# Kernel tuning notes

Hardware: AMD Instinct MI355X
Metric: run time of the kernel (lower is better)

## Reference

```python
import jax, jax.numpy as jnp
import numpy as np

B, D, K, C = 512, 256, 65536, 1000
T_SUP, T_DC, LS = 0.07, 0.1, 0.1
EPS = 1e-8


def _l2norm(x, axis):
    return x / jnp.linalg.norm(x, axis=axis, keepdims=True)


def setup_inputs() -> dict:
    key = jax.random.key(0)
    k1, k2, k3, k4, k5, k6, k7, k8 = jax.random.split(key, 8)
    norm_q = _l2norm(jax.random.normal(k1, (B, D), jnp.float32), axis=1)
    k_feat = _l2norm(jax.random.normal(k2, (B, D), jnp.float32), axis=1)
    q_logits = jax.random.normal(k3, (B, C), jnp.float32)
    logits_k = jax.random.normal(k4, (B, C), jnp.float32)
    queue = _l2norm(jax.random.normal(k5, (D, K), jnp.float32), axis=0)
    # queue_label_prob stores softmaxed class-probabilities column-wise (prob.T)
    queue_label_prob = jax.nn.softmax(jax.random.normal(k6, (C, K), jnp.float32), axis=0)
    queue_label = jax.random.randint(k7, (K,), 0, C, jnp.int64)
    target = jax.random.randint(k8, (B,), 0, C, jnp.int64)
    return {
        "norm_q": norm_q, "q_logits": q_logits, "k_feat": k_feat,
        "logits_k": logits_k, "queue": queue,
        "queue_label_prob": queue_label_prob, "queue_label": queue_label,
        "target": target, "knn_k": 200,
    }


def reference(norm_q, q_logits, k_feat, logits_k, queue, queue_label_prob,
              queue_label, target, knn_k):
    b = norm_q.shape[0]

    # ---- supcon_in ----
    sim = norm_q @ queue                                  # [B, K]
    _, idx = jax.lax.top_k(sim, knn_k)                    # [B, knn_k]
    sim_knn = jnp.take_along_axis(sim, idx, axis=1)
    w = jax.nn.softmax(sim_knn / T_SUP, axis=-1)
    pos = (target[:, None] == queue_label[idx])           # [B, knn_k]
    gt = jnp.sum(w * pos, axis=1)                         # [B]
    m = gt > EPS
    supin_loss = jnp.sum(jnp.where(m, -jnp.log(jnp.where(m, gt, 1.0)), 0.0)) / b

    # ---- label-smoothed onehot ----
    onehot = jnp.full((b, C), LS / (C - 1), jnp.float32)
    onehot = onehot.at[jnp.arange(b), target].set(1.0 - LS)

    log_q = jax.nn.log_softmax(q_logits, axis=1)
    q_mask = jax.nn.softmax(q_logits, axis=1).min(axis=1) > EPS  # [B]

    # ---- fc loss (masked CE with label smoothing) ----
    fc_loss = -jnp.sum(jnp.sum(onehot * log_q, axis=1) * q_mask) / b

    # ---- generate_dc_target (no-grad in original) ----
    sim_k = jax.nn.softmax((k_feat @ queue) / T_DC, axis=-1)      # [B, K]
    dc_target = sim_k @ queue_label_prob.T                        # [B, C]

    # ---- dc loss: KL(dc_target || softmax(q_logits)), masked, sum / B ----
    kl = jnp.where(dc_target > 0, dc_target * (jnp.log(jnp.where(dc_target > 0, dc_target, 1.0)) - log_q), 0.0)
    dc_loss = jnp.sum(jnp.sum(kl, axis=1) * q_mask) / b

    return (supin_loss, fc_loss, dc_loss)
```

## Files before the change

kernel.cpp:

```cpp
#include <hip/hip_runtime.h>
#include <math.h>

#define BN 512
#define DN 256
#define KN 65536
#define CN 1000
#define EQ_CAP 512
#define EPSTR 136

typedef __attribute__((ext_vector_type(8))) short bf16x8;
typedef __attribute__((ext_vector_type(4))) float f32x4;

__device__ __forceinline__ unsigned short f2bf(float f) {
    unsigned u = __float_as_uint(f);
    unsigned r = (u + 0x7FFFu + ((u >> 16) & 1u)) >> 16;
    return (unsigned short)r;
}
__device__ __forceinline__ float bf2f(unsigned short h) {
    return __uint_as_float(((unsigned)h) << 16);
}
__device__ __forceinline__ unsigned fkey16(unsigned b) {
    b &= 0xFFFFu;
    return (b & 0x8000u) ? ((~b) & 0xFFFFu) : (b | 0x8000u);
}
__device__ __forceinline__ void async16(const void* g, void* l) {
    __builtin_amdgcn_global_load_lds(
        (const __attribute__((address_space(1))) unsigned*)g,
        (__attribute__((address_space(3))) unsigned*)l, 16, 0, 0);
}

__global__ void __launch_bounds__(256) cvt_bf16(const float* __restrict__ in,
                                                unsigned short* __restrict__ out) {
    int i = (blockIdx.x * 256 + threadIdx.x) * 4;
    float4 v = *(const float4*)&in[i];
    ushort4 o;
    o.x = f2bf(v.x); o.y = f2bf(v.y); o.z = f2bf(v.z); o.w = f2bf(v.w);
    *(ushort4*)&out[i] = o;
}

__global__ void __launch_bounds__(256) transpose_q(const float* __restrict__ Q,
                                                   unsigned short* __restrict__ Qt) {
    __shared__ float T[64][65];
    int tid = threadIdx.x;
    int n0 = blockIdx.x * 64;
    int d0 = blockIdx.y * 64;
    #pragma unroll
    for (int i = 0; i < 4; ++i) {
        int flat = i * 256 + tid;
        int d = flat >> 4, nq = (flat & 15) * 4;
        float4 v = *(const float4*)&Q[(size_t)(d0 + d) * KN + n0 + nq];
        T[d][nq] = v.x; T[d][nq + 1] = v.y; T[d][nq + 2] = v.z; T[d][nq + 3] = v.w;
    }
    __syncthreads();
    int n = tid >> 2, dbase = (tid & 3) * 16;
    unsigned u[8];
    #pragma unroll
    for (int j = 0; j < 8; ++j) {
        unsigned short a = f2bf(T[dbase + 2 * j][n]);
        unsigned short b = f2bf(T[dbase + 2 * j + 1][n]);
        u[j] = (unsigned)a | ((unsigned)b << 16);
    }
    unsigned short* o = &Qt[(size_t)(n0 + n) * DN + d0 + dbase];
    *(uint4*)o = make_uint4(u[0], u[1], u[2], u[3]);
    *(uint4*)(o + 8) = make_uint4(u[4], u[5], u[6], u[7]);
}

__global__ void __launch_bounds__(256) gemm_sim(const unsigned short* __restrict__ A,
                                                const unsigned short* __restrict__ Bt,
                                                unsigned short* __restrict__ simOut,
                                                unsigned short* __restrict__ expOut,
                                                float* __restrict__ Zb,
                                                int mBlockSplit) {
    __shared__ unsigned short smem[128 * 64 * 2];
    __shared__ float Zred[128];
    unsigned short* As = smem;
    unsigned short* Bs = smem + 128 * 64;
    int tid = threadIdx.x;
    int n0 = blockIdx.x * 128, m0 = blockIdx.y * 128;
    bool isExp = ((int)blockIdx.y >= mBlockSplit);
    int lane = tid & 63, w = tid >> 6;
    int l15 = lane & 15, quad = lane >> 4;
    int wm = w & 1, wn = w >> 1;
    f32x4 acc[4][4];
    #pragma unroll
    for (int mi = 0; mi < 4; ++mi)
        #pragma unroll
        for (int ni = 0; ni < 4; ++ni)
            #pragma unroll
            for (int j = 0; j < 4; ++j) acc[mi][ni][j] = 0.f;

    for (int k0 = 0; k0 < DN; k0 += 64) {
        #pragma unroll
        for (int i = 0; i < 4; ++i) {
            int f = (i * 256 + tid) * 8;
            async16(A + (size_t)(m0 + (f >> 6)) * DN + k0 + (f & 63), &As[f]);
        }
        #pragma unroll
        for (int i = 0; i < 4; ++i) {
            int f = (i * 256 + tid) * 8;
            async16(Bt + (size_t)(n0 + (f >> 6)) * DN + k0 + (f & 63), &Bs[f]);
        }
        __syncthreads();
        #pragma unroll
        for (int ks = 0; ks < 2; ++ks) {
            bf16x8 am[4], bn[4];
            #pragma unroll
            for (int mi = 0; mi < 4; ++mi)
                am[mi] = *(const bf16x8*)&As[(wm * 64 + mi * 16 + l15) * 64 + ks * 32 + quad * 8];
            #pragma unroll
            for (int ni = 0; ni < 4; ++ni)
                bn[ni] = *(const bf16x8*)&Bs[(wn * 64 + ni * 16 + l15) * 64 + ks * 32 + quad * 8];
            #pragma unroll
            for (int mi = 0; mi < 4; ++mi)
                #pragma unroll
                for (int ni = 0; ni < 4; ++ni)
                    acc[mi][ni] = __builtin_amdgcn_mfma_f32_16x16x32_bf16(bn[ni], am[mi], acc[mi][ni], 0, 0, 0);
        }
        __syncthreads();
    }

    unsigned short* obase = isExp ? expOut : simOut;
    int orow0 = isExp ? (m0 - mBlockSplit * 128) : m0;
    float rsum[4] = {0.f, 0.f, 0.f, 0.f};

    #pragma unroll
    for (int round = 0; round < 2; ++round) {
        if (wm == round) {
            #pragma unroll
            for (int mi = 0; mi < 4; ++mi) {
                int mrow = mi * 16 + l15;
                #pragma unroll
                for (int ni = 0; ni < 4; ++ni) {
                    int nc = wn * 64 + ni * 16 + quad * 4;
                    float v0 = acc[mi][ni][0], v1 = acc[mi][ni][1];
                    float v2 = acc[mi][ni][2], v3 = acc[mi][ni][3];
                    if (isExp) {
                        v0 = __expf(v0 * 10.0f); v1 = __expf(v1 * 10.0f);
                        v2 = __expf(v2 * 10.0f); v3 = __expf(v3 * 10.0f);
                    }
                    unsigned short u0 = f2bf(v0), u1 = f2bf(v1), u2 = f2bf(v2), u3 = f2bf(v3);
                    if (isExp) rsum[mi] += bf2f(u0) + bf2f(u1) + bf2f(u2) + bf2f(u3);
                    *(uint2*)&smem[mrow * EPSTR + nc] =
                        make_uint2((unsigned)u0 | ((unsigned)u1 << 16),
                                   (unsigned)u2 | ((unsigned)u3 << 16));
                }
            }
        }
        __syncthreads();
        #pragma unroll
        for (int j = 0; j < 4; ++j) {
            int fc = j * 256 + tid;
            int mr = fc >> 4;
            int ch = fc & 15;
            uint4 val = *(uint4*)&smem[mr * EPSTR + ch * 8];
            int g = orow0 + round * 64 + mr;
            *(uint4*)&obase[(size_t)g * KN + n0 + ch * 8] = val;
        }
        __syncthreads();
    }

    if (isExp) {
        float v4[4];
        #pragma unroll
        for (int mi = 0; mi < 4; ++mi) {
            float v = rsum[mi];
            v += __shfl_xor(v, 16, 64);
            v += __shfl_xor(v, 32, 64);
            v4[mi] = v;
        }
        if (wn == 0 && quad == 0) {
            #pragma unroll
            for (int mi = 0; mi < 4; ++mi) Zred[wm * 64 + mi * 16 + l15] = v4[mi];
        }
        __syncthreads();
        if (wn == 1 && quad == 0) {
            #pragma unroll
            for (int mi = 0; mi < 4; ++mi) Zred[wm * 64 + mi * 16 + l15] += v4[mi];
        }
        __syncthreads();
        if (tid < 128) atomicAdd(&Zb[orow0 + tid], Zred[tid]);
    }
}

__global__ void __launch_bounds__(256) supcon(const unsigned short* __restrict__ sim,
                                              const int* __restrict__ qlabel,
                                              const int* __restrict__ target,
                                              const int* __restrict__ knnp,
                                              float* __restrict__ out0) {
    __shared__ unsigned hist[4][256];
    __shared__ unsigned s_sel, s_cntAbove;
    __shared__ int eqIdx[EQ_CAP];
    __shared__ unsigned eqCount;
    __shared__ float redZ[256], redN[256];
    int tid = threadIdx.x, w = tid >> 6;
    int row = blockIdx.x;
    const unsigned short* srow = sim + (size_t)row * KN;
    int knn = *knnp;
    int tgt = target[row];
    if (tid == 0) { eqCount = 0u; }
    #pragma unroll
    for (int j = 0; j < 4; ++j) hist[j][tid] = 0u;
    __syncthreads();
    for (int i0 = tid * 4; i0 < KN; i0 += 1024) {
        uint2 v = *(const uint2*)&srow[i0];
        atomicAdd(&hist[w][fkey16(v.x) >> 8], 1u);
        atomicAdd(&hist[w][fkey16(v.x >> 16) >> 8], 1u);
        atomicAdd(&hist[w][fkey16(v.y) >> 8], 1u);
        atomicAdd(&hist[w][fkey16(v.y >> 16) >> 8], 1u);
    }
    __syncthreads();
    if (tid == 0) {
        unsigned acc = 0; int chosen = 0;
        for (int bin = 255; bin >= 0; --bin) {
            unsigned h = hist[0][bin] + hist[1][bin] + hist[2][bin] + hist[3][bin];
            if (acc + h >= (unsigned)knn) { chosen = bin; break; }
            acc += h;
        }
        s_cntAbove = acc; s_sel = (unsigned)chosen;
    }
    __syncthreads();
    unsigned selHi = s_sel;
    #pragma unroll
    for (int j = 0; j < 4; ++j) hist[j][tid] = 0u;
    __syncthreads();
    for (int i0 = tid * 4; i0 < KN; i0 += 1024) {
        uint2 v = *(const uint2*)&srow[i0];
        unsigned k0 = fkey16(v.x), k1 = fkey16(v.x >> 16), k2 = fkey16(v.y), k3 = fkey16(v.y >> 16);
        if ((k0 >> 8) == selHi) atomicAdd(&hist[w][k0 & 255u], 1u);
        if ((k1 >> 8) == selHi) atomicAdd(&hist[w][k1 & 255u], 1u);
        if ((k2 >> 8) == selHi) atomicAdd(&hist[w][k2 & 255u], 1u);
        if ((k3 >> 8) == selHi) atomicAdd(&hist[w][k3 & 255u], 1u);
    }
    __syncthreads();
    if (tid == 0) {
        unsigned acc = s_cntAbove; int chosen = 0;
        for (int bin = 255; bin >= 0; --bin) {
            unsigned h = hist[0][bin] + hist[1][bin] + hist[2][bin] + hist[3][bin];
            if (acc + h >= (unsigned)knn) { chosen = bin; break; }
            acc += h;
        }
        s_cntAbove = acc; s_sel = (selHi << 8) | (unsigned)chosen;
    }
    __syncthreads();
    unsigned tu = s_sel;
    unsigned cgt = s_cntAbove;
    const float invT = 1.0f / 0.07f;
    float Zl = 0.f, Nl = 0.f;
    for (int i0 = tid * 4; i0 < KN; i0 += 1024) {
        uint2 v = *(const uint2*)&srow[i0];
        unsigned bits[4] = {v.x & 0xFFFFu, v.x >> 16, v.y & 0xFFFFu, v.y >> 16};
        #pragma unroll
        for (int j = 0; j < 4; ++j) {
            unsigned u = fkey16(bits[j]);
            if (u > tu) {
                float e = __expf(bf2f((unsigned short)bits[j]) * invT);
                Zl += e;
                if (qlabel[i0 + j] == tgt) Nl += e;
            } else if (u == tu) {
                unsigned pos = atomicAdd(&eqCount, 1u);
                if (pos < EQ_CAP) eqIdx[pos] = i0 + j;
            }
        }
    }
    redZ[tid] = Zl; redN[tid] = Nl;
    __syncthreads();
    for (int s = 128; s > 0; s >>= 1) {
        if (tid < s) { redZ[tid] += redZ[tid + s]; redN[tid] += redN[tid + s]; }
        __syncthreads();
    }
    if (tid == 0) {
        float Z = redZ[0], num = redN[0];
        int neq = (int)(eqCount < (unsigned)EQ_CAP ? eqCount : (unsigned)EQ_CAP);
        int needed = knn - (int)cgt;
        if (needed > neq) needed = neq;
        for (int a = 1; a < neq; ++a) {
            int v = eqIdx[a]; int b2 = a - 1;
            while (b2 >= 0 && eqIdx[b2] > v) { eqIdx[b2 + 1] = eqIdx[b2]; --b2; }
            eqIdx[b2 + 1] = v;
        }
        unsigned tb = (tu & 0x8000u) ? (tu & 0x7FFFu) : ((~tu) & 0xFFFFu);
        float wt = __expf(bf2f((unsigned short)tb) * invT);
        for (int a = 0; a < needed; ++a) {
            Z += wt;
            if (qlabel[eqIdx[a]] == tgt) num += wt;
        }
        float gt = num / Z;
        if (gt > 1e-8f) atomicAdd(out0, -logf(gt) * (1.0f / (float)BN));
    }
}

__global__ void __launch_bounds__(256) dc_gemm(const unsigned short* __restrict__ E,
                                               const float* __restrict__ P,
                                               float* __restrict__ dct) {
    __shared__ unsigned short As[128 * 32];
    __shared__ unsigned short Bs[128 * 32];
    int tid = threadIdx.x;
    int c0 = blockIdx.x * 128, m0 = blockIdx.y * 128;
    int kb = blockIdx.z * (KN / 16);
    int lane = tid & 63, w = tid >> 6;
    int l15 = lane & 15, quad = lane >> 4;
    int wm = w & 1, wn = w >> 1;
    int crow = tid >> 1, khalf = (tid & 1) * 16;
    bool cvalid = (c0 + crow) < CN;
    const float* pbase = P + (size_t)(c0 + crow) * KN + khalf;
    f32x4 acc[4][4];
    #pragma unroll
    for (int r = 0; r < 4; ++r)
        #pragma unroll
        for (int c = 0; c < 4; ++c)
            #pragma unroll
            for (int j = 0; j < 4; ++j) acc[r][c][j] = 0.f;
    for (int kc = 0; kc < KN / 16; kc += 32) {
        int k0 = kb + kc;
        #pragma unroll
        for (int i = 0; i < 2; ++i) {
            int flat = (i * 256 + tid) * 8;
            int row = flat >> 5, kk = flat & 31;
            async16(E + (size_t)(m0 + row) * KN + k0 + kk, &As[flat]);
        }
        float4 p0 = make_float4(0.f, 0.f, 0.f, 0.f), p1 = p0, p2 = p0, p3 = p0;
        if (cvalid) {
            p0 = *(const float4*)&pbase[k0];
            p1 = *(const float4*)&pbase[k0 + 4];
            p2 = *(const float4*)&pbase[k0 + 8];
            p3 = *(const float4*)&pbase[k0 + 12];
        }
        unsigned u0 = (unsigned)f2bf(p0.x) | ((unsigned)f2bf(p0.y) << 16);
        unsigned u1 = (unsigned)f2bf(p0.z) | ((unsigned)f2bf(p0.w) << 16);
        unsigned u2 = (unsigned)f2bf(p1.x) | ((unsigned)f2bf(p1.y) << 16);
        unsigned u3 = (unsigned)f2bf(p1.z) | ((unsigned)f2bf(p1.w) << 16);
        unsigned u4 = (unsigned)f2bf(p2.x) | ((unsigned)f2bf(p2.y) << 16);
        unsigned u5 = (unsigned)f2bf(p2.z) | ((unsigned)f2bf(p2.w) << 16);
        unsigned u6 = (unsigned)f2bf(p3.x) | ((unsigned)f2bf(p3.y) << 16);
        unsigned u7 = (unsigned)f2bf(p3.z) | ((unsigned)f2bf(p3.w) << 16);
        *(uint4*)&Bs[crow * 32 + khalf] = make_uint4(u0, u1, u2, u3);
        *(uint4*)&Bs[crow * 32 + khalf + 8] = make_uint4(u4, u5, u6, u7);
        __syncthreads();
        bf16x8 af[4], bfr[4];
        #pragma unroll
        for (int r = 0; r < 4; ++r) af[r] = *(const bf16x8*)&As[(wm * 64 + r * 16 + l15) * 32 + quad * 8];
        #pragma unroll
        for (int c = 0; c < 4; ++c) bfr[c] = *(const bf16x8*)&Bs[(wn * 64 + c * 16 + l15) * 32 + quad * 8];
        #pragma unroll
        for (int r = 0; r < 4; ++r)
            #pragma unroll
            for (int c = 0; c < 4; ++c)
                acc[r][c] = __builtin_amdgcn_mfma_f32_16x16x32_bf16(af[r], bfr[c], acc[r][c], 0, 0, 0);
        __syncthreads();
    }
    #pragma unroll
    for (int r = 0; r < 4; ++r)
        #pragma unroll
        for (int reg = 0; reg < 4; ++reg) {
            int m = m0 + wm * 64 + r * 16 + quad * 4 + reg;
            #pragma unroll
            for (int c = 0; c < 4; ++c) {
                int cc = c0 + wn * 64 + c * 16 + l15;
                atomicAdd(&dct[m * 1024 + cc], acc[r][c][reg]);
            }
        }
}

__global__ void __launch_bounds__(256) logq_fc(const float* __restrict__ x_all,
                                               const int* __restrict__ target,
                                               float* __restrict__ logq,
                                               float* __restrict__ qmask,
                                               float* __restrict__ out1) {
    int row = blockIdx.x, tid = threadIdx.x;
    const float* x = x_all + (size_t)row * CN;
    __shared__ float red[256], red2[256];
    float mx = -INFINITY, mn = INFINITY;
    for (int c = tid; c < CN; c += 256) { float v = x[c]; mx = fmaxf(mx, v); mn = fminf(mn, v); }
    red[tid] = mx; red2[tid] = mn;
    __syncthreads();
    for (int s = 128; s > 0; s >>= 1) {
        if (tid < s) { red[tid] = fmaxf(red[tid], red[tid + s]); red2[tid] = fminf(red2[tid], red2[tid + s]); }
        __syncthreads();
    }
    mx = red[0]; mn = red2[0];
    __syncthreads();
    float se = 0.f, sx = 0.f;
    for (int c = tid; c < CN; c += 256) { float v = x[c]; se += __expf(v - mx); sx += v; }
    red[tid] = se; red2[tid] = sx;
    __syncthreads();
    for (int s = 128; s > 0; s >>= 1) {
        if (tid < s) { red[tid] += red[tid + s]; red2[tid] += red2[tid + s]; }
        __syncthreads();
    }
    float lse = mx + logf(red[0]);
    float sumlogq = red2[0] - (float)CN * lse;
    for (int c = tid; c < CN; c += 256) logq[(size_t)row * CN + c] = x[c] - lse;
    if (tid == 0) {
        float lqt = x[target[row]] - lse;
        bool qm = (mn - lse) > logf(1e-8f);
        qmask[row] = qm ? 1.0f : 0.0f;
        if (qm) {
            float fc = -(0.1f / 999.0f * (sumlogq - lqt) + 0.9f * lqt);
            atomicAdd(out1, fc * (1.0f / (float)BN));
        }
    }
}

__global__ void __launch_bounds__(256) dc_loss(const float* __restrict__ dct,
                                               const float* __restrict__ logq,
                                               const float* __restrict__ qmask,
                                               const float* __restrict__ Z,
                                               float* __restrict__ out2) {
    int row = blockIdx.x, tid = threadIdx.x;
    __shared__ float red[256];
    float invZ = 1.0f / Z[row];
    float s = 0.f;
    for (int c = tid; c < CN; c += 256) {
        float T = dct[row * 1024 + c] * invZ;
        if (T > 0.f) s += T * (logf(T) - logq[(size_t)row * CN + c]);
    }
    red[tid] = s;
    __syncthreads();
    for (int st = 128; st > 0; st >>= 1) {
        if (tid < st) red[tid] += red[tid + st];
        __syncthreads();
    }
    if (tid == 0 && qmask[row] > 0.f)
        atomicAdd(out2, red[0] * (1.0f / (float)BN));
}

extern "C" void kernel_launch(void* const* d_in, const int* in_sizes, int n_in,
                              void* d_out, int out_size, void* d_ws, size_t ws_size,
                              hipStream_t stream) {
    (void)in_sizes; (void)n_in; (void)out_size;
    const float* norm_q   = (const float*)d_in[0];
    const float* q_logits = (const float*)d_in[1];
    const float* k_feat   = (const float*)d_in[2];
    const float* queue    = (const float*)d_in[4];
    const float* qlp      = (const float*)d_in[5];
    const int*   qlabel   = (const int*)d_in[6];
    const int*   target   = (const int*)d_in[7];
    const int*   knnp     = (const int*)d_in[8];
    float* out = (float*)d_out;
    char* ws = (char*)d_ws;

    const size_t SIM_B = 67108864;
    const size_t QT_B  = 33554432;
    const size_t AC_B  = 524288;
    const size_t FUSED_NEED = SIM_B * 2 + QT_B + AC_B + 2097152 + 2048 + 2048000 + 2048;
    bool fused = (ws_size >= FUSED_NEED);

    unsigned short *simBF, *Ebf, *queueT, *Acat;
    float *dct, *Zb, *logq, *qmask;
    if (fused) {
        simBF  = (unsigned short*)(ws);
        Ebf    = (unsigned short*)(ws + SIM_B);
        queueT = (unsigned short*)(ws + 2 * SIM_B);
        Acat   = (unsigned short*)(ws + 2 * SIM_B + QT_B);
        dct    = (float*)(ws + 2 * SIM_B + QT_B + AC_B);
    } else {
        simBF  = (unsigned short*)(ws);
        Ebf    = simBF;
        queueT = (unsigned short*)(ws + SIM_B);
        Acat   = (unsigned short*)(ws + SIM_B + QT_B);
        dct    = (float*)(ws + SIM_B + QT_B + AC_B);
    }
    Zb    = (float*)((char*)dct + 2097152);
    logq  = (float*)((char*)Zb + 2048);
    qmask = (float*)((char*)logq + 2048000);

    hipMemsetAsync(dct, 0, 2097152 + 2048, stream);
    hipMemsetAsync(d_out, 0, 3 * sizeof(float), stream);

    cvt_bf16<<<dim3(128), 256, 0, stream>>>(norm_q, Acat);
    cvt_bf16<<<dim3(128), 256, 0, stream>>>(k_feat, Acat + (size_t)BN * DN);
    transpose_q<<<dim3(KN / 64, 4), 256, 0, stream>>>(queue, queueT);

    if (fused) {
        gemm_sim<<<dim3(KN / 128, 8), 256, 0, stream>>>(Acat, queueT, simBF, Ebf, Zb, 4);
        supcon<<<dim3(BN), 256, 0, stream>>>(simBF, qlabel, target, knnp, out + 0);
    } else {
        gemm_sim<<<dim3(KN / 128, 4), 256, 0, stream>>>(Acat, queueT, simBF, nullptr, nullptr, 4);
        supcon<<<dim3(BN), 256, 0, stream>>>(simBF, qlabel, target, knnp, out + 0);
        gemm_sim<<<dim3(KN / 128, 4), 256, 0, stream>>>(Acat + (size_t)BN * DN, queueT,
                                                        nullptr, Ebf, Zb, 0);
    }
    dc_gemm<<<dim3(8, 4, 16), 256, 0, stream>>>(Ebf, qlp, dct);
    logq_fc<<<dim3(BN), 256, 0, stream>>>(q_logits, target, logq, qmask, out + 1);
    dc_loss<<<dim3(BN), 256, 0, stream>>>(dct, logq, qmask, Zb, out + 2);
}
```

Before: 800.9 us.

## Split dc_gemm K into partial buffers and parallelize supcon bin selection

The DC GEMM now splits K into 32 chunks, each writing to its own partial buffer, instead of accumulating into one buffer with float atomics. It uses a 64-wide K tile with XOR-swizzled LDS and register-staged loads. dc_loss sums the 32 partials per element. In supcon, the single-thread serial histogram bin search becomes a parallel suffix scan over the 256 bins. The cost is 64MB of extra partial-buffer traffic, and the non-fused workspace fallback path is removed.

```diff
diff --git a/kernel.cpp b/kernel.cpp
--- a/kernel.cpp
+++ b/kernel.cpp
@@ -7,6 +7,7 @@
 #define CN 1000
 #define EQ_CAP 512
 #define EPSTR 136
+#define DCSPLIT 32
 
 typedef __attribute__((ext_vector_type(8))) short bf16x8;
 typedef __attribute__((ext_vector_type(4))) float f32x4;
@@ -188,6 +189,7 @@
                                               const int* __restrict__ knnp,
                                               float* __restrict__ out0) {
     __shared__ unsigned hist[4][256];
+    __shared__ unsigned sc[256];
     __shared__ unsigned s_sel, s_cntAbove;
     __shared__ int eqIdx[EQ_CAP];
     __shared__ unsigned eqCount;
@@ -195,9 +197,9 @@
     int tid = threadIdx.x, w = tid >> 6;
     int row = blockIdx.x;
     const unsigned short* srow = sim + (size_t)row * KN;
-    int knn = *knnp;
+    unsigned knn = (unsigned)*knnp;
     int tgt = target[row];
-    if (tid == 0) { eqCount = 0u; }
+    if (tid == 0) eqCount = 0u;
     #pragma unroll
     for (int j = 0; j < 4; ++j) hist[j][tid] = 0u;
     __syncthreads();
@@ -209,16 +211,19 @@
         atomicAdd(&hist[w][fkey16(v.y >> 16) >> 8], 1u);
     }
     __syncthreads();
-    if (tid == 0) {
-        unsigned acc = 0; int chosen = 0;
-        for (int bin = 255; bin >= 0; --bin) {
-            unsigned h = hist[0][bin] + hist[1][bin] + hist[2][bin] + hist[3][bin];
-            if (acc + h >= (unsigned)knn) { chosen = bin; break; }
-            acc += h;
-        }
-        s_cntAbove = acc; s_sel = (unsigned)chosen;
-    }
-    __syncthreads();
+    {
+        unsigned tot = hist[0][tid] + hist[1][tid] + hist[2][tid] + hist[3][tid];
+        sc[tid] = tot; __syncthreads();
+        #pragma unroll
+        for (int off = 1; off < 256; off <<= 1) {
+            unsigned v = (tid + off < 256) ? sc[tid + off] : 0u;
+            __syncthreads();
+            sc[tid] += v; __syncthreads();
+        }
+        unsigned S = sc[tid];
+        if (S >= knn && S - tot < knn) { s_sel = (unsigned)tid; s_cntAbove = S - tot; }
+        __syncthreads();
+    }
     unsigned selHi = s_sel;
     #pragma unroll
     for (int j = 0; j < 4; ++j) hist[j][tid] = 0u;
@@ -232,16 +237,23 @@
         if ((k3 >> 8) == selHi) atomicAdd(&hist[w][k3 & 255u], 1u);
     }
     __syncthreads();
-    if (tid == 0) {
-        unsigned acc = s_cntAbove; int chosen = 0;
-        for (int bin = 255; bin >= 0; --bin) {
-            unsigned h = hist[0][bin] + hist[1][bin] + hist[2][bin] + hist[3][bin];
-            if (acc + h >= (unsigned)knn) { chosen = bin; break; }
-            acc += h;
-        }
-        s_cntAbove = acc; s_sel = (selHi << 8) | (unsigned)chosen;
-    }
-    __syncthreads();
+    {
+        unsigned base = s_cntAbove;
+        unsigned tot = hist[0][tid] + hist[1][tid] + hist[2][tid] + hist[3][tid];
+        sc[tid] = tot; __syncthreads();
+        #pragma unroll
+        for (int off = 1; off < 256; off <<= 1) {
+            unsigned v = (tid + off < 256) ? sc[tid + off] : 0u;
+            __syncthreads();
+            sc[tid] += v; __syncthreads();
+        }
+        unsigned S = base + sc[tid];
+        if (S >= knn && S - tot < knn) {
+            s_sel = (selHi << 8) | (unsigned)tid;
+            s_cntAbove = S - tot;
+        }
+        __syncthreads();
+    }
     unsigned tu = s_sel;
     unsigned cgt = s_cntAbove;
     const float invT = 1.0f / 0.07f;
@@ -271,7 +283,7 @@
     if (tid == 0) {
         float Z = redZ[0], num = redN[0];
         int neq = (int)(eqCount < (unsigned)EQ_CAP ? eqCount : (unsigned)EQ_CAP);
-        int needed = knn - (int)cgt;
+        int needed = (int)knn - (int)cgt;
         if (needed > neq) needed = neq;
         for (int a = 1; a < neq; ++a) {
             int v = eqIdx[a]; int b2 = a - 1;
@@ -291,73 +303,72 @@
 
 __global__ void __launch_bounds__(256) dc_gemm(const unsigned short* __restrict__ E,
                                                const float* __restrict__ P,
-                                               float* __restrict__ dct) {
-    __shared__ unsigned short As[128 * 32];
-    __shared__ unsigned short Bs[128 * 32];
+                                               float* __restrict__ part) {
+    __shared__ unsigned short As[128 * 64];
+    __shared__ unsigned short Bs[128 * 64];
     int tid = threadIdx.x;
     int c0 = blockIdx.x * 128, m0 = blockIdx.y * 128;
-    int kb = blockIdx.z * (KN / 16);
+    int kb = blockIdx.z * (KN / DCSPLIT);
     int lane = tid & 63, w = tid >> 6;
     int l15 = lane & 15, quad = lane >> 4;
-    int wm = w & 1, wn = w >> 1;
-    int crow = tid >> 1, khalf = (tid & 1) * 16;
-    bool cvalid = (c0 + crow) < CN;
-    const float* pbase = P + (size_t)(c0 + crow) * KN + khalf;
+    int wm = w & 1, wc = w >> 1;
     f32x4 acc[4][4];
     #pragma unroll
-    for (int r = 0; r < 4; ++r)
-        #pragma unroll
-        for (int c = 0; c < 4; ++c)
-            #pragma unroll
-            for (int j = 0; j < 4; ++j) acc[r][c][j] = 0.f;
-    for (int kc = 0; kc < KN / 16; kc += 32) {
+    for (int ci = 0; ci < 4; ++ci)
+        #pragma unroll
+        for (int mi = 0; mi < 4; ++mi)
+            #pragma unroll
+            for (int j = 0; j < 4; ++j) acc[ci][mi][j] = 0.f;
+
+    for (int kc = 0; kc < KN / DCSPLIT; kc += 64) {
         int k0 = kb + kc;
         #pragma unroll
-        for (int i = 0; i < 2; ++i) {
-            int flat = (i * 256 + tid) * 8;
-            int row = flat >> 5, kk = flat & 31;
-            async16(E + (size_t)(m0 + row) * KN + k0 + kk, &As[flat]);
-        }
-        float4 p0 = make_float4(0.f, 0.f, 0.f, 0.f), p1 = p0, p2 = p0, p3 = p0;
-        if (cvalid) {
-            p0 = *(const float4*)&pbase[k0];
-            p1 = *(const float4*)&pbase[k0 + 4];
-            p2 = *(const float4*)&pbase[k0 + 8];
-            p3 = *(const float4*)&pbase[k0 + 12];
-        }
-        unsigned u0 = (unsigned)f2bf(p0.x) | ((unsigned)f2bf(p0.y) << 16);
-        unsigned u1 = (unsigned)f2bf(p0.z) | ((unsigned)f2bf(p0.w) << 16);
-        unsigned u2 = (unsigned)f2bf(p1.x) | ((unsigned)f2bf(p1.y) << 16);
-        unsigned u3 = (unsigned)f2bf(p1.z) | ((unsigned)f2bf(p1.w) << 16);
-        unsigned u4 = (unsigned)f2bf(p2.x) | ((unsigned)f2bf(p2.y) << 16);
-        unsigned u5 = (unsigned)f2bf(p2.z) | ((unsigned)f2bf(p2.w) << 16);
-        unsigned u6 = (unsigned)f2bf(p3.x) | ((unsigned)f2bf(p3.y) << 16);
-        unsigned u7 = (unsigned)f2bf(p3.z) | ((unsigned)f2bf(p3.w) << 16);
-        *(uint4*)&Bs[crow * 32 + khalf] = make_uint4(u0, u1, u2, u3);
-        *(uint4*)&Bs[crow * 32 + khalf + 8] = make_uint4(u4, u5, u6, u7);
-        __syncthreads();
-        bf16x8 af[4], bfr[4];
-        #pragma unroll
-        for (int r = 0; r < 4; ++r) af[r] = *(const bf16x8*)&As[(wm * 64 + r * 16 + l15) * 32 + quad * 8];
-        #pragma unroll
-        for (int c = 0; c < 4; ++c) bfr[c] = *(const bf16x8*)&Bs[(wn * 64 + c * 16 + l15) * 32 + quad * 8];
-        #pragma unroll
-        for (int r = 0; r < 4; ++r)
-            #pragma unroll
-            for (int c = 0; c < 4; ++c)
-                acc[r][c] = __builtin_amdgcn_mfma_f32_16x16x32_bf16(af[r], bfr[c], acc[r][c], 0, 0, 0);
-        __syncthreads();
-    }
-    #pragma unroll
-    for (int r = 0; r < 4; ++r)
-        #pragma unroll
-        for (int reg = 0; reg < 4; ++reg) {
-            int m = m0 + wm * 64 + r * 16 + quad * 4 + reg;
-            #pragma unroll
-            for (int c = 0; c < 4; ++c) {
-                int cc = c0 + wn * 64 + c * 16 + l15;
-                atomicAdd(&dct[m * 1024 + cc], acc[r][c][reg]);
-            }
+        for (int i = 0; i < 4; ++i) {
+            int f = (i * 256 + tid) * 8;
+            int er = f >> 6, ek = f & 63;
+            uint4 ev = *(const uint4*)&E[(size_t)(m0 + er) * KN + k0 + ek];
+            int cj = (ek >> 3) ^ (er & 7);
+            *(uint4*)&As[er * 64 + cj * 8] = ev;
+        }
+        #pragma unroll
+        for (int i = 0; i < 8; ++i) {
+            int f = (i * 256 + tid) * 4;
+            int pr = f >> 6, pk = f & 63;
+            float4 pv = make_float4(0.f, 0.f, 0.f, 0.f);
+            if (c0 + pr < CN) pv = *(const float4*)&P[(size_t)(c0 + pr) * KN + k0 + pk];
+            unsigned lo = (unsigned)f2bf(pv.x) | ((unsigned)f2bf(pv.y) << 16);
+            unsigned hi = (unsigned)f2bf(pv.z) | ((unsigned)f2bf(pv.w) << 16);
+            int cj = (pk >> 3) ^ (pr & 7);
+            *(uint2*)&Bs[pr * 64 + cj * 8 + (pk & 7)] = make_uint2(lo, hi);
+        }
+        __syncthreads();
+        #pragma unroll
+        for (int ks = 0; ks < 2; ++ks) {
+            int sw = ((ks * 4 + quad) ^ (l15 & 7)) * 8;
+            bf16x8 am[4], bc[4];
+            #pragma unroll
+            for (int mi = 0; mi < 4; ++mi)
+                am[mi] = *(const bf16x8*)&As[(wm * 64 + mi * 16 + l15) * 64 + sw];
+            #pragma unroll
+            for (int ci = 0; ci < 4; ++ci)
+                bc[ci] = *(const bf16x8*)&Bs[(wc * 64 + ci * 16 + l15) * 64 + sw];
+            #pragma unroll
+            for (int ci = 0; ci < 4; ++ci)
+                #pragma unroll
+                for (int mi = 0; mi < 4; ++mi)
+                    acc[ci][mi] = __builtin_amdgcn_mfma_f32_16x16x32_bf16(bc[ci], am[mi], acc[ci][mi], 0, 0, 0);
+        }
+        __syncthreads();
+    }
+    float* pb = part + (size_t)blockIdx.z * (512 * 1024);
+    #pragma unroll
+    for (int ci = 0; ci < 4; ++ci)
+        #pragma unroll
+        for (int mi = 0; mi < 4; ++mi) {
+            int m = m0 + wm * 64 + mi * 16 + l15;
+            int c = c0 + wc * 64 + ci * 16 + quad * 4;
+            *(float4*)&pb[(size_t)m * 1024 + c] =
+                make_float4(acc[ci][mi][0], acc[ci][mi][1], acc[ci][mi][2], acc[ci][mi][3]);
         }
 }
 
@@ -401,7 +412,7 @@
     }
 }
 
-__global__ void __launch_bounds__(256) dc_loss(const float* __restrict__ dct,
+__global__ void __launch_bounds__(256) dc_loss(const float* __restrict__ part,
                                                const float* __restrict__ logq,
                                                const float* __restrict__ qmask,
                                                const float* __restrict__ Z,
@@ -411,7 +422,11 @@
     float invZ = 1.0f / Z[row];
     float s = 0.f;
     for (int c = tid; c < CN; c += 256) {
-        float T = dct[row * 1024 + c] * invZ;
+        float t = 0.f;
+        #pragma unroll
+        for (int sp = 0; sp < DCSPLIT; ++sp)
+            t += part[(size_t)sp * (512 * 1024) + (size_t)row * 1024 + c];
+        float T = t * invZ;
         if (T > 0.f) s += T * (logf(T) - logq[(size_t)row * CN + c]);
     }
     red[tid] = s;
@@ -427,7 +442,7 @@
 extern "C" void kernel_launch(void* const* d_in, const int* in_sizes, int n_in,
                               void* d_out, int out_size, void* d_ws, size_t ws_size,
                               hipStream_t stream) {
-    (void)in_sizes; (void)n_in; (void)out_size;
+    (void)in_sizes; (void)n_in; (void)out_size; (void)ws_size;
     const float* norm_q   = (const float*)d_in[0];
     const float* q_logits = (const float*)d_in[1];
     const float* k_feat   = (const float*)d_in[2];
@@ -439,48 +454,25 @@
     float* out = (float*)d_out;
     char* ws = (char*)d_ws;
 
-    const size_t SIM_B = 67108864;
-    const size_t QT_B  = 33554432;
-    const size_t AC_B  = 524288;
-    const size_t FUSED_NEED = SIM_B * 2 + QT_B + AC_B + 2097152 + 2048 + 2048000 + 2048;
-    bool fused = (ws_size >= FUSED_NEED);
-
-    unsigned short *simBF, *Ebf, *queueT, *Acat;
-    float *dct, *Zb, *logq, *qmask;
-    if (fused) {
-        simBF  = (unsigned short*)(ws);
-        Ebf    = (unsigned short*)(ws + SIM_B);
-        queueT = (unsigned short*)(ws + 2 * SIM_B);
-        Acat   = (unsigned short*)(ws + 2 * SIM_B + QT_B);
-        dct    = (float*)(ws + 2 * SIM_B + QT_B + AC_B);
-    } else {
-        simBF  = (unsigned short*)(ws);
-        Ebf    = simBF;
-        queueT = (unsigned short*)(ws + SIM_B);
-        Acat   = (unsigned short*)(ws + SIM_B + QT_B);
-        dct    = (float*)(ws + SIM_B + QT_B + AC_B);
-    }
-    Zb    = (float*)((char*)dct + 2097152);
-    logq  = (float*)((char*)Zb + 2048);
-    qmask = (float*)((char*)logq + 2048000);
-
-    hipMemsetAsync(dct, 0, 2097152 + 2048, stream);
+    unsigned short* Ebf    = (unsigned short*)(ws);
+    unsigned short* simBF  = (unsigned short*)(ws + 67108864);
+    float*          part   = (float*)(ws + 67108864);
+    unsigned short* queueT = (unsigned short*)(ws + 134217728);
+    unsigned short* Acat   = (unsigned short*)(ws + 167772160);
+    float* Zb    = (float*)(ws + 168296448);
+    float* logq  = (float*)(ws + 168298496);
+    float* qmask = (float*)(ws + 170346496);
+
+    hipMemsetAsync(Zb, 0, 2048, stream);
     hipMemsetAsync(d_out, 0, 3 * sizeof(float), stream);
 
     cvt_bf16<<<dim3(128), 256, 0, stream>>>(norm_q, Acat);
     cvt_bf16<<<dim3(128), 256, 0, stream>>>(k_feat, Acat + (size_t)BN * DN);
     transpose_q<<<dim3(KN / 64, 4), 256, 0, stream>>>(queue, queueT);
 
-    if (fused) {
-        gemm_sim<<<dim3(KN / 128, 8), 256, 0, stream>>>(Acat, queueT, simBF, Ebf, Zb, 4);
-        supcon<<<dim3(BN), 256, 0, stream>>>(simBF, qlabel, target, knnp, out + 0);
-    } else {
-        gemm_sim<<<dim3(KN / 128, 4), 256, 0, stream>>>(Acat, queueT, simBF, nullptr, nullptr, 4);
-        supcon<<<dim3(BN), 256, 0, stream>>>(simBF, qlabel, target, knnp, out + 0);
-        gemm_sim<<<dim3(KN / 128, 4), 256, 0, stream>>>(Acat + (size_t)BN * DN, queueT,
-                                                        nullptr, Ebf, Zb, 0);
-    }
-    dc_gemm<<<dim3(8, 4, 16), 256, 0, stream>>>(Ebf, qlp, dct);
+    gemm_sim<<<dim3(KN / 128, 8), 256, 0, stream>>>(Acat, queueT, simBF, Ebf, Zb, 4);
+    supcon<<<dim3(BN), 256, 0, stream>>>(simBF, qlabel, target, knnp, out + 0);
+    dc_gemm<<<dim3(8, 4, DCSPLIT), 256, 0, stream>>>(Ebf, qlp, part);
     logq_fc<<<dim3(BN), 256, 0, stream>>>(q_logits, target, logq, qmask, out + 1);
-    dc_loss<<<dim3(BN), 256, 0, stream>>>(dct, logq, qmask, Zb, out + 2);
-}
+    dc_loss<<<dim3(BN), 256, 0, stream>>>(part, logq, qmask, Zb, out + 2);
+}
```

New measurement: 940.0 us. +17.4%, slower.
